# Kernel optimization log

Measured on AMD Instinct MI355X. Metric: run time of the kernel, lower is better.

Reference implementation:

```python
import jax, jax.numpy as jnp
import numpy as np

N = 50000   # nodes
E = 150000  # edges
G = 256     # graphs in batch
H0, H1, H2, H3 = 8, 128, 256, 512


def _lin(key, fi, fo):
    return jax.random.normal(key, (fi, fo), dtype=jnp.float32) * (1.0 / np.sqrt(fi))


def setup_inputs() -> dict:
    key = jax.random.key(0)
    ks = jax.random.split(key, 12)
    x = jax.random.normal(ks[0], (N, H0), dtype=jnp.float32)
    edge_index = jax.random.randint(ks[1], (2, E), 0, N)
    edge_weight = jax.random.uniform(ks[2], (E,), dtype=jnp.float32)
    batch = jnp.sort(jax.random.randint(ks[3], (N,), 0, G))
    return {
        'x': x, 'edge_index': edge_index, 'edge_weight': edge_weight, 'batch': batch,
        'W1': _lin(ks[4], H0, H1), 'b1': jnp.zeros((H1,), jnp.float32),
        'W2': _lin(ks[5], H1, H2), 'b2': jnp.zeros((H2,), jnp.float32),
        'W3': _lin(ks[6], H2, H3), 'b3': jnp.zeros((H3,), jnp.float32),
        'Wfc': _lin(ks[7], H3, 1), 'bfc': jnp.zeros((1,), jnp.float32),
    }


def _gcn_conv(h, W, b, src, dst, ew, n):
    # h: [N, Fin] -> [N, Fout]; symmetric GCN normalization (self-loops already in src/dst/ew)
    h = h @ W                                             # [N, Fout]
    deg = jax.ops.segment_sum(ew, dst, num_segments=n)    # [N]
    dinv = jnp.where(deg > 0, jax.lax.rsqrt(deg), 0.0)
    norm = dinv[src] * ew * dinv[dst]                     # [E+N]
    msgs = h[src] * norm[:, None]                         # gather + scale
    out = jax.ops.segment_sum(msgs, dst, num_segments=n)  # scatter-add
    return out + b


def reference(x, edge_index, edge_weight, batch, W1, b1, W2, b2, W3, b3, Wfc, bfc):
    n = x.shape[0]
    loop = jnp.arange(n)
    src = jnp.concatenate([edge_index[0], loop])
    dst = jnp.concatenate([edge_index[1], loop])
    ew = jnp.concatenate([edge_weight, jnp.ones((n,), edge_weight.dtype)])

    h1 = jax.nn.relu(_gcn_conv(x, W1, b1, src, dst, ew, n))
    h2 = jax.nn.relu(_gcn_conv(h1, W2, b2, src, dst, ew, n))
    h3 = jax.nn.relu(_gcn_conv(h2, W3, b3, src, dst, ew, n))

    # global mean pool over graphs
    sums = jax.ops.segment_sum(h3, batch, num_segments=G)              # [G, H3]
    cnt = jax.ops.segment_sum(jnp.ones((n,), h3.dtype), batch, num_segments=G)
    pooled = sums / jnp.maximum(cnt, 1.0)[:, None]

    return jax.nn.sigmoid(pooled @ Wfc + bfc)              # [G, 1]
```

## Files before the change

### kernel.cpp

```cpp
#include <hip/hip_runtime.h>
#include <math.h>

typedef __attribute__((ext_vector_type(8))) short short8;
typedef __attribute__((ext_vector_type(4))) float floatx4;


__device__ __forceinline__ unsigned short f2bf(float f) {
    unsigned int u = __float_as_uint(f);
    unsigned int r = (u + 0x7fffu + ((u >> 16) & 1u)) >> 16;
    return (unsigned short)r;
}
__device__ __forceinline__ float bfu_lo(unsigned int u) {
    return __uint_as_float(u << 16);
}
__device__ __forceinline__ float bfu_hi(unsigned int u) {
    return __uint_as_float(u & 0xffff0000u);
}


__global__ void k_init_wt(float* __restrict__ deg, int* __restrict__ cnt,
                          int* __restrict__ cursor, int N,
                          const float* __restrict__ W2, unsigned short* __restrict__ WT2,
                          int K2, int F2,
                          const float* __restrict__ W3, unsigned short* __restrict__ WT3,
                          int K3, int F3) {
    int i = blockIdx.x * blockDim.x + threadIdx.x;
    if (i < N) { deg[i] = 1.0f; cnt[i] = 0; cursor[i] = 0; }
    int n2 = K2 * F2;
    if (i < n2) {
        int k = i / F2, n = i % F2;
        WT2[(size_t)n * K2 + k] = f2bf(W2[i]);
    } else {
        int j = i - n2;
        if (j < K3 * F3) {
            int k = j / F3, n = j % F3;
            WT3[(size_t)n * K3 + k] = f2bf(W3[j]);
        }
    }
}

__global__ void k_hist_deg(const int* __restrict__ dst, const float* __restrict__ ew,
                           float* __restrict__ deg, int* __restrict__ cnt, int E) {
    int e = blockIdx.x * blockDim.x + threadIdx.x;
    if (e < E) {
        int d = dst[e];
        atomicAdd(&deg[d], ew[e]);
        atomicAdd(&cnt[d], 1);
    }
}

__global__ __launch_bounds__(256) void k_dinv_scana(float* __restrict__ deg,
                                                    const int* __restrict__ cnt,
                                                    int* __restrict__ bsum, int N) {
    int b = blockIdx.x, t = threadIdx.x;
    int base = b * 1024 + t * 4;
    int s = 0;
#pragma unroll
    for (int j = 0; j < 4; ++j) {
        int i = base + j;
        if (i < N) { deg[i] = rsqrtf(deg[i]); s += cnt[i]; }
    }
    __shared__ int sh[256];
    sh[t] = s; __syncthreads();
    for (int st = 128; st > 0; st >>= 1) { if (t < st) sh[t] += sh[t + st]; __syncthreads(); }
    if (t == 0) bsum[b] = sh[0];
}

__global__ __launch_bounds__(256) void k_scan_c(const int* __restrict__ cnt,
                                                const int* __restrict__ bsum,
                                                int* __restrict__ row_start, int N, int nb) {
    int b = blockIdx.x, t = threadIdx.x;
    __shared__ int sh[256];
    __shared__ int boffs;

    if (t < 64) {
        int s = 0;
        for (int i = t; i < b; i += 64) s += bsum[i];
#pragma unroll
        for (int off = 32; off > 0; off >>= 1) s += __shfl_down(s, off);
        if (t == 0) boffs = s;
    }
    __syncthreads();

    int base = b * 1024 + t * 4;
    int v[4]; int s = 0;
#pragma unroll
    for (int j = 0; j < 4; ++j) { int i = base + j; v[j] = (i < N) ? cnt[i] : 0; s += v[j]; }
    sh[t] = s; __syncthreads();
    for (int off = 1; off < 256; off <<= 1) {
        int x = (t >= off) ? sh[t - off] : 0;
        __syncthreads();
        sh[t] += x;
        __syncthreads();
    }
    int excl = sh[t] - s + boffs;
#pragma unroll
    for (int j = 0; j < 4; ++j) {
        int i = base + j;
        if (i < N) row_start[i] = excl;
        excl += v[j];
        if (i == N - 1) row_start[N] = excl;
    }
}

__global__ void k_scatter_norm(const int* __restrict__ src, const int* __restrict__ dst,
                               const float* __restrict__ ew, const float* __restrict__ dinv,
                               const int* __restrict__ row_start, int* __restrict__ cursor,
                               int* __restrict__ esrc, float* __restrict__ enorm, int E) {
    int e = blockIdx.x * blockDim.x + threadIdx.x;
    if (e >= E) return;
    int d = dst[e], s = src[e];
    int pos = row_start[d] + atomicAdd(&cursor[d], 1);
    esrc[pos] = s;
    enorm[pos] = dinv[s] * ew[e] * dinv[d];
}


__global__ __launch_bounds__(256) void k_l1_gemm(
    const float* __restrict__ x, const float* __restrict__ dinv,
    const int* __restrict__ esrc, const float* __restrict__ enorm,
    const int* __restrict__ row_start, const float* __restrict__ W1,
    const float* __restrict__ b1, unsigned short* __restrict__ h1, int N) {
    __shared__ float As[8][132];
    __shared__ float Bs[8][128];

    int tid = threadIdx.x;
    int bm = blockIdx.x * 128;

#pragma unroll
    for (int i = tid; i < 1024; i += 256) Bs[i >> 7][i & 127] = W1[i];

    if (tid < 128) {
        int n = bm + tid;
        float a[8] = {0, 0, 0, 0, 0, 0, 0, 0};
        if (n < N) {
            float dv = dinv[n];
            float dv2 = dv * dv;
            float4 v0 = *(const float4*)&x[(size_t)n * 8];
            float4 v1 = *(const float4*)&x[(size_t)n * 8 + 4];
            a[0] = v0.x * dv2; a[1] = v0.y * dv2; a[2] = v0.z * dv2; a[3] = v0.w * dv2;
            a[4] = v1.x * dv2; a[5] = v1.y * dv2; a[6] = v1.z * dv2; a[7] = v1.w * dv2;
            int j1 = row_start[n + 1];
            for (int j = row_start[n]; j < j1; ++j) {
                int s = esrc[j];
                float w = enorm[j];
                float4 u0 = *(const float4*)&x[(size_t)s * 8];
                float4 u1 = *(const float4*)&x[(size_t)s * 8 + 4];
                a[0] += w * u0.x; a[1] += w * u0.y; a[2] += w * u0.z; a[3] += w * u0.w;
                a[4] += w * u1.x; a[5] += w * u1.y; a[6] += w * u1.z; a[7] += w * u1.w;
            }
        }
#pragma unroll
        for (int k = 0; k < 8; ++k) As[k][tid] = a[k];
    }
    __syncthreads();

    int tx = tid & 15;
    int ty = tid >> 4;
    float acc[8][8];
#pragma unroll
    for (int i = 0; i < 8; ++i)
#pragma unroll
        for (int j = 0; j < 8; ++j) acc[i][j] = 0.f;

#pragma unroll
    for (int k = 0; k < 8; ++k) {
        float a[8], b[8];
        float4 a0 = *(const float4*)&As[k][ty * 4];
        float4 a1 = *(const float4*)&As[k][ty * 4 + 64];
        float4 b0 = *(const float4*)&Bs[k][tx * 4];
        float4 b1 = *(const float4*)&Bs[k][tx * 4 + 64];
        a[0] = a0.x; a[1] = a0.y; a[2] = a0.z; a[3] = a0.w;
        a[4] = a1.x; a[5] = a1.y; a[6] = a1.z; a[7] = a1.w;
        b[0] = b0.x; b[1] = b0.y; b[2] = b0.z; b[3] = b0.w;
        b[4] = b1.x; b[5] = b1.y; b[6] = b1.z; b[7] = b1.w;
#pragma unroll
        for (int i = 0; i < 8; ++i)
#pragma unroll
            for (int j = 0; j < 8; ++j) acc[i][j] += a[i] * b[j];
    }

    float4 bi0 = *(const float4*)&b1[tx * 4];
    float4 bi1 = *(const float4*)&b1[tx * 4 + 64];
    float bb[8] = {bi0.x, bi0.y, bi0.z, bi0.w, bi1.x, bi1.y, bi1.z, bi1.w};
#pragma unroll
    for (int i = 0; i < 8; ++i) {
        int gm = bm + ((i < 4) ? (ty * 4 + i) : (64 + ty * 4 + i - 4));
        if (gm >= N) continue;
        ushort4 v0, v1;
        v0.x = f2bf(fmaxf(acc[i][0] + bb[0], 0.f));
        v0.y = f2bf(fmaxf(acc[i][1] + bb[1], 0.f));
        v0.z = f2bf(fmaxf(acc[i][2] + bb[2], 0.f));
        v0.w = f2bf(fmaxf(acc[i][3] + bb[3], 0.f));
        v1.x = f2bf(fmaxf(acc[i][4] + bb[4], 0.f));
        v1.y = f2bf(fmaxf(acc[i][5] + bb[5], 0.f));
        v1.z = f2bf(fmaxf(acc[i][6] + bb[6], 0.f));
        v1.w = f2bf(fmaxf(acc[i][7] + bb[7], 0.f));
        *(ushort4*)&h1[(size_t)gm * 128 + tx * 4] = v0;
        *(ushort4*)&h1[(size_t)gm * 128 + tx * 4 + 64] = v1;
    }
}


__global__ void k_agg_bf(const unsigned short* __restrict__ h, const float* __restrict__ dinv,
                         const int* __restrict__ esrc, const float* __restrict__ enorm,
                         const int* __restrict__ row_start,
                         unsigned short* __restrict__ A,
                         int N, int Mpad, int F, int osh) {
    int p = blockIdx.x * blockDim.x + threadIdx.x;
    int oct = F >> 3;
    if (p >= Mpad * oct) return;
    int n = p >> osh;
    int fo = (p & (oct - 1)) << 3;
    size_t oidx = (size_t)n * F + fo;
    if (n >= N) {
        *(uint4*)&A[oidx] = make_uint4(0, 0, 0, 0);
        return;
    }
    float dv = dinv[n];
    float dv2 = dv * dv;
    uint4 hv = *(const uint4*)&h[oidx];
    float s0 = bfu_lo(hv.x) * dv2, s1 = bfu_hi(hv.x) * dv2;
    float s2 = bfu_lo(hv.y) * dv2, s3 = bfu_hi(hv.y) * dv2;
    float s4 = bfu_lo(hv.z) * dv2, s5 = bfu_hi(hv.z) * dv2;
    float s6 = bfu_lo(hv.w) * dv2, s7 = bfu_hi(hv.w) * dv2;
    int j1 = row_start[n + 1];
    for (int j = row_start[n]; j < j1; ++j) {
        int s = esrc[j];
        float w = enorm[j];
        uint4 nv = *(const uint4*)&h[(size_t)s * F + fo];
        s0 += w * bfu_lo(nv.x); s1 += w * bfu_hi(nv.x);
        s2 += w * bfu_lo(nv.y); s3 += w * bfu_hi(nv.y);
        s4 += w * bfu_lo(nv.z); s5 += w * bfu_hi(nv.z);
        s6 += w * bfu_lo(nv.w); s7 += w * bfu_hi(nv.w);
    }
    uint4 o;
    o.x = (unsigned int)f2bf(s0) | ((unsigned int)f2bf(s1) << 16);
    o.y = (unsigned int)f2bf(s2) | ((unsigned int)f2bf(s3) << 16);
    o.z = (unsigned int)f2bf(s4) | ((unsigned int)f2bf(s5) << 16);
    o.w = (unsigned int)f2bf(s6) | ((unsigned int)f2bf(s7) << 16);
    *(uint4*)&A[oidx] = o;
}


template <int EPI>
__global__ __launch_bounds__(256, 4) void k_gemm_async(
    const unsigned short* __restrict__ A, const unsigned short* __restrict__ B,
    const float* __restrict__ bias, unsigned short* __restrict__ C,
    const float* __restrict__ Wfc, float* __restrict__ part,
    int M, int Mpad, int K, int Fout, int nbsh) {
    __shared__ __align__(16) unsigned short smem[8192];

    int tid = threadIdx.x, wave = tid >> 6, lane = tid & 63;
    int quad = lane >> 4, r = lane & 15;

    int P = blockIdx.x;
    int r8 = P & 7;
    int q = P >> 3;
    int bnIdx = q & ((1 << nbsh) - 1);
    int g = ((q >> nbsh) << 3) + r8;
    int bm = g * 128, bn = bnIdx * 128;
    int wm = (wave & 1) * 64, wn = (wave >> 1) * 64;

    const unsigned short* gsrc[2] = {A, B};
    const int rb[2] = {bm, bn};

    floatx4 acc[4][4] = {};

    for (int k0 = 0; k0 < K; k0 += 32) {
#pragma unroll
        for (int t = 0; t < 2; ++t) {
#pragma unroll
            for (int i = 0; i < 2; ++i) {
                int qc = wave * 2 + i;
                int idx = qc * 64 + lane;
                int row = idx >> 2, kofs = (idx & 3) << 3;
                const unsigned short* gptr = gsrc[t] + ((size_t)(rb[t] + row) * K + k0 + kofs);
                unsigned short* l = &smem[t * 4096 + qc * 512];
                __builtin_amdgcn_global_load_lds(
                    (const __attribute__((address_space(1))) void*)gptr,
                    (__attribute__((address_space(3))) void*)l, 16, 0, 0);
            }
        }
        __syncthreads();

        short8 ah[4];
#pragma unroll
        for (int mt = 0; mt < 4; ++mt) {
            int m = wm + mt * 16 + r;
            ah[mt] = *(const short8*)&smem[m * 32 + quad * 8];
        }
#pragma unroll
        for (int nt = 0; nt < 4; ++nt) {
            int n = wn + nt * 16 + r;
            short8 bh = *(const short8*)&smem[4096 + n * 32 + quad * 8];
#pragma unroll
            for (int mt = 0; mt < 4; ++mt)
                acc[mt][nt] = __builtin_amdgcn_mfma_f32_16x16x32_bf16(ah[mt], bh, acc[mt][nt], 0, 0, 0);
        }
        __syncthreads();
    }

    float bv[4];
#pragma unroll
    for (int nt = 0; nt < 4; ++nt) bv[nt] = bias[bn + wn + nt * 16 + r];

    if (EPI == 0) {
        float* eps = (float*)&smem[0] + wave * 1024;
#pragma unroll
        for (int mt = 0; mt < 4; ++mt) {
#pragma unroll
            for (int nt = 0; nt < 4; ++nt)
#pragma unroll
                for (int reg = 0; reg < 4; ++reg)
                    eps[(quad * 4 + reg) * 64 + nt * 16 + r] =
                        fmaxf(acc[mt][nt][reg] + bv[nt], 0.f);
#pragma unroll
            for (int i = 0; i < 4; ++i) {
                int fl = i * 64 + lane;
                int ri = fl >> 4, c4 = fl & 15;
                float4 v = *(const float4*)&eps[ri * 64 + c4 * 4];
                int gm = bm + wm + mt * 16 + ri;
                if (gm < M)
                    *(ushort4*)&C[(size_t)gm * Fout + bn + wn + c4 * 4] =
                        make_ushort4(f2bf(v.x), f2bf(v.y), f2bf(v.z), f2bf(v.w));
            }
        }
    } else {
        float* rowsum = (float*)&smem[0];
        if (tid < 128) rowsum[tid] = 0.f;
        __syncthreads();
        float wf[4];
#pragma unroll
        for (int nt = 0; nt < 4; ++nt) wf[nt] = Wfc[bn + wn + nt * 16 + r];
#pragma unroll
        for (int mt = 0; mt < 4; ++mt)
#pragma unroll
            for (int reg = 0; reg < 4; ++reg) {
                float v = 0.f;
#pragma unroll
                for (int nt = 0; nt < 4; ++nt)
                    v += fmaxf(acc[mt][nt][reg] + bv[nt], 0.f) * wf[nt];
                v += __shfl_xor(v, 1);
                v += __shfl_xor(v, 2);
                v += __shfl_xor(v, 4);
                v += __shfl_xor(v, 8);
                if (r == 0) atomicAdd(&rowsum[wm + mt * 16 + quad * 4 + reg], v);
            }
        __syncthreads();
        if (tid < 128) part[(size_t)bnIdx * Mpad + bm + tid] = rowsum[tid];
    }
}


__global__ __launch_bounds__(256) void k_pool2(const float* __restrict__ part,
                                               const int* __restrict__ batch,
                                               const float* __restrict__ bfc,
                                               float* __restrict__ out,
                                               int N, int Mpad, int nchunks, int G) {
    int g = (int)((blockIdx.x * blockDim.x + threadIdx.x) >> 6);
    int lane = threadIdx.x & 63;
    if (g >= G) return;
    int lo = 0, hi = N;
    while (lo < hi) { int m = (lo + hi) >> 1; if (batch[m] < g) lo = m + 1; else hi = m; }
    int start = lo;
    hi = N;
    while (lo < hi) { int m = (lo + hi) >> 1; if (batch[m] < g + 1) lo = m + 1; else hi = m; }
    int end = lo;
    float s = 0.f;
    for (int i = start + lane; i < end; i += 64) {
        float t = 0.f;
        for (int c = 0; c < nchunks; ++c) t += part[(size_t)c * Mpad + i];
        s += t;
    }
#pragma unroll
    for (int off = 32; off > 0; off >>= 1) s += __shfl_down(s, off);
    if (lane == 0) {
        float c = (float)(end - start);
        if (c < 1.f) c = 1.f;
        float z = s / c + bfc[0];
        out[g] = 1.f / (1.f + expf(-z));
    }
}


static inline int cdiv(int a, int b) { return (a + b - 1) / b; }

extern "C" void kernel_launch(void* const* d_in, const int* in_sizes, int n_in,
                              void* d_out, int out_size, void* d_ws, size_t ws_size,
                              hipStream_t stream) {
    const float* x   = (const float*)d_in[0];
    const int*   ei  = (const int*)d_in[1];
    const float* ew  = (const float*)d_in[2];
    const int*   bat = (const int*)d_in[3];
    const float* W1  = (const float*)d_in[4];
    const float* b1  = (const float*)d_in[5];
    const float* W2  = (const float*)d_in[6];
    const float* b2  = (const float*)d_in[7];
    const float* W3  = (const float*)d_in[8];
    const float* b3  = (const float*)d_in[9];
    const float* Wfc = (const float*)d_in[10];
    const float* bfc = (const float*)d_in[11];
    float* out = (float*)d_out;

    const int N  = in_sizes[3];
    const int E  = in_sizes[2];
    const int H1 = in_sizes[5];
    const int H2 = in_sizes[7];
    const int H3 = in_sizes[9];
    const int G  = out_size;
    const int Mpad = cdiv(N, 1024) * 1024;
    const int Npad4 = (N + 4) & ~3;

    const int* srcv = ei;
    const int* dstv = ei + E;

    char* p = (char*)d_ws;
    float* dinv      = (float*)p; p += (size_t)N * 4;
    int*   cnt       = (int*)p;   p += (size_t)N * 4;
    int*   cursor    = (int*)p;   p += (size_t)N * 4;
    int*   bsum      = (int*)p;   p += 256 * 4;
    int*   row_start = (int*)p;   p += (size_t)Npad4 * 4;
    int*   esrc      = (int*)p;   p += (size_t)E * 4;
    float* enorm     = (float*)p; p += (size_t)E * 4;
    float* part      = (float*)p; p += (size_t)(H3 / 128) * Mpad * 4;
    unsigned short* WT2 = (unsigned short*)p; p += (size_t)H1 * H2 * 2;
    unsigned short* WT3 = (unsigned short*)p; p += (size_t)H2 * H3 * 2;
    unsigned short* Abf = (unsigned short*)p; p += (size_t)Mpad * H2 * 2;
    unsigned short* h1  = (unsigned short*)p; p += (size_t)Mpad * H1 * 2;
    unsigned short* h2  = (unsigned short*)p; p += (size_t)Mpad * H2 * 2;

    int initTot = H1 * H2 + H2 * H3;
    if (initTot < N) initTot = N;
    k_init_wt<<<cdiv(initTot, 256), 256, 0, stream>>>(dinv, cnt, cursor, N,
                                                      W2, WT2, H1, H2, W3, WT3, H2, H3);
    k_hist_deg<<<cdiv(E, 256), 256, 0, stream>>>(dstv, ew, dinv, cnt, E);
    int nb = cdiv(N, 1024);
    k_dinv_scana<<<nb, 256, 0, stream>>>(dinv, cnt, bsum, N);
    k_scan_c<<<nb, 256, 0, stream>>>(cnt, bsum, row_start, N, nb);
    k_scatter_norm<<<cdiv(E, 256), 256, 0, stream>>>(srcv, dstv, ew, dinv, row_start,
                                                     cursor, esrc, enorm, E);

    k_l1_gemm<<<cdiv(N, 128), 256, 0, stream>>>(x, dinv, esrc, enorm, row_start, W1, b1, h1, N);

    k_agg_bf<<<cdiv(Mpad * (H1 / 8), 256), 256, 0, stream>>>(
        h1, dinv, esrc, enorm, row_start, Abf, N, Mpad, H1, __builtin_ctz(H1) - 3);
    k_gemm_async<0><<<(Mpad / 128) * (H2 / 128), 256, 0, stream>>>(
        Abf, WT2, b2, h2, nullptr, nullptr, N, Mpad, H1, H2, __builtin_ctz(H2 / 128));

    k_agg_bf<<<cdiv(Mpad * (H2 / 8), 256), 256, 0, stream>>>(
        h2, dinv, esrc, enorm, row_start, Abf, N, Mpad, H2, __builtin_ctz(H2) - 3);
    k_gemm_async<1><<<(Mpad / 128) * (H3 / 128), 256, 0, stream>>>(
        Abf, WT3, b3, nullptr, Wfc, part, N, Mpad, H2, H3, __builtin_ctz(H3 / 128));

    k_pool2<<<cdiv(G * 64, 256), 256, 0, stream>>>(part, bat, bfc, out, N, Mpad, H3 / 128, G);
}
```

Before: 225.0 us.

## Fuse mean-pool into final GEMM epilogue and unroll edge gathers by four

```diff
diff --git a/kernel.cpp b/kernel.cpp
--- a/kernel.cpp
+++ b/kernel.cpp
@@ -23,9 +23,12 @@
                           const float* __restrict__ W2, unsigned short* __restrict__ WT2,
                           int K2, int F2,
                           const float* __restrict__ W3, unsigned short* __restrict__ WT3,
-                          int K3, int F3) {
+                          int K3, int F3,
+                          float* __restrict__ gsum, int* __restrict__ done, int G) {
     int i = blockIdx.x * blockDim.x + threadIdx.x;
     if (i < N) { deg[i] = 1.0f; cnt[i] = 0; cursor[i] = 0; }
+    if (i < G) gsum[i] = 0.f;
+    if (i == 0) *done = 0;
     int n2 = K2 * F2;
     if (i < n2) {
         int k = i / F2, n = i % F2;
@@ -140,14 +143,32 @@
             float4 v1 = *(const float4*)&x[(size_t)n * 8 + 4];
             a[0] = v0.x * dv2; a[1] = v0.y * dv2; a[2] = v0.z * dv2; a[3] = v0.w * dv2;
             a[4] = v1.x * dv2; a[5] = v1.y * dv2; a[6] = v1.z * dv2; a[7] = v1.w * dv2;
-            int j1 = row_start[n + 1];
-            for (int j = row_start[n]; j < j1; ++j) {
-                int s = esrc[j];
-                float w = enorm[j];
-                float4 u0 = *(const float4*)&x[(size_t)s * 8];
-                float4 u1 = *(const float4*)&x[(size_t)s * 8 + 4];
-                a[0] += w * u0.x; a[1] += w * u0.y; a[2] += w * u0.z; a[3] += w * u0.w;
-                a[4] += w * u1.x; a[5] += w * u1.y; a[6] += w * u1.z; a[7] += w * u1.w;
+            int j0 = row_start[n], j1 = row_start[n + 1];
+            for (int b = j0; b < j1; b += 4) {
+                int i1 = (b + 1 < j1) ? b + 1 : b;
+                int i2 = (b + 2 < j1) ? b + 2 : b;
+                int i3 = (b + 3 < j1) ? b + 3 : b;
+                float w0 = enorm[b];
+                float w1 = (b + 1 < j1) ? enorm[i1] : 0.f;
+                float w2 = (b + 2 < j1) ? enorm[i2] : 0.f;
+                float w3 = (b + 3 < j1) ? enorm[i3] : 0.f;
+                int s0 = esrc[b], s1 = esrc[i1], s2 = esrc[i2], s3 = esrc[i3];
+                float4 p0 = *(const float4*)&x[(size_t)s0 * 8];
+                float4 q0 = *(const float4*)&x[(size_t)s0 * 8 + 4];
+                float4 p1 = *(const float4*)&x[(size_t)s1 * 8];
+                float4 q1 = *(const float4*)&x[(size_t)s1 * 8 + 4];
+                float4 p2 = *(const float4*)&x[(size_t)s2 * 8];
+                float4 q2 = *(const float4*)&x[(size_t)s2 * 8 + 4];
+                float4 p3 = *(const float4*)&x[(size_t)s3 * 8];
+                float4 q3 = *(const float4*)&x[(size_t)s3 * 8 + 4];
+                a[0] += w0 * p0.x + w1 * p1.x + w2 * p2.x + w3 * p3.x;
+                a[1] += w0 * p0.y + w1 * p1.y + w2 * p2.y + w3 * p3.y;
+                a[2] += w0 * p0.z + w1 * p1.z + w2 * p2.z + w3 * p3.z;
+                a[3] += w0 * p0.w + w1 * p1.w + w2 * p2.w + w3 * p3.w;
+                a[4] += w0 * q0.x + w1 * q1.x + w2 * q2.x + w3 * q3.x;
+                a[5] += w0 * q0.y + w1 * q1.y + w2 * q2.y + w3 * q3.y;
+                a[6] += w0 * q0.z + w1 * q1.z + w2 * q2.z + w3 * q3.z;
+                a[7] += w0 * q0.w + w1 * q1.w + w2 * q2.w + w3 * q3.w;
             }
         }
 #pragma unroll
@@ -224,15 +245,28 @@
     float s2 = bfu_lo(hv.y) * dv2, s3 = bfu_hi(hv.y) * dv2;
     float s4 = bfu_lo(hv.z) * dv2, s5 = bfu_hi(hv.z) * dv2;
     float s6 = bfu_lo(hv.w) * dv2, s7 = bfu_hi(hv.w) * dv2;
-    int j1 = row_start[n + 1];
-    for (int j = row_start[n]; j < j1; ++j) {
-        int s = esrc[j];
-        float w = enorm[j];
-        uint4 nv = *(const uint4*)&h[(size_t)s * F + fo];
-        s0 += w * bfu_lo(nv.x); s1 += w * bfu_hi(nv.x);
-        s2 += w * bfu_lo(nv.y); s3 += w * bfu_hi(nv.y);
-        s4 += w * bfu_lo(nv.z); s5 += w * bfu_hi(nv.z);
-        s6 += w * bfu_lo(nv.w); s7 += w * bfu_hi(nv.w);
+    int j0 = row_start[n], j1 = row_start[n + 1];
+    for (int b = j0; b < j1; b += 4) {
+        int i1 = (b + 1 < j1) ? b + 1 : b;
+        int i2 = (b + 2 < j1) ? b + 2 : b;
+        int i3 = (b + 3 < j1) ? b + 3 : b;
+        float w0 = enorm[b];
+        float w1 = (b + 1 < j1) ? enorm[i1] : 0.f;
+        float w2 = (b + 2 < j1) ? enorm[i2] : 0.f;
+        float w3 = (b + 3 < j1) ? enorm[i3] : 0.f;
+        int e0 = esrc[b], e1 = esrc[i1], e2 = esrc[i2], e3 = esrc[i3];
+        uint4 r0 = *(const uint4*)&h[(size_t)e0 * F + fo];
+        uint4 r1 = *(const uint4*)&h[(size_t)e1 * F + fo];
+        uint4 r2 = *(const uint4*)&h[(size_t)e2 * F + fo];
+        uint4 r3 = *(const uint4*)&h[(size_t)e3 * F + fo];
+        s0 += w0 * bfu_lo(r0.x) + w1 * bfu_lo(r1.x) + w2 * bfu_lo(r2.x) + w3 * bfu_lo(r3.x);
+        s1 += w0 * bfu_hi(r0.x) + w1 * bfu_hi(r1.x) + w2 * bfu_hi(r2.x) + w3 * bfu_hi(r3.x);
+        s2 += w0 * bfu_lo(r0.y) + w1 * bfu_lo(r1.y) + w2 * bfu_lo(r2.y) + w3 * bfu_lo(r3.y);
+        s3 += w0 * bfu_hi(r0.y) + w1 * bfu_hi(r1.y) + w2 * bfu_hi(r2.y) + w3 * bfu_hi(r3.y);
+        s4 += w0 * bfu_lo(r0.z) + w1 * bfu_lo(r1.z) + w2 * bfu_lo(r2.z) + w3 * bfu_lo(r3.z);
+        s5 += w0 * bfu_hi(r0.z) + w1 * bfu_hi(r1.z) + w2 * bfu_hi(r2.z) + w3 * bfu_hi(r3.z);
+        s6 += w0 * bfu_lo(r0.w) + w1 * bfu_lo(r1.w) + w2 * bfu_lo(r2.w) + w3 * bfu_lo(r3.w);
+        s7 += w0 * bfu_hi(r0.w) + w1 * bfu_hi(r1.w) + w2 * bfu_hi(r2.w) + w3 * bfu_hi(r3.w);
     }
     uint4 o;
     o.x = (unsigned int)f2bf(s0) | ((unsigned int)f2bf(s1) << 16);
@@ -247,9 +281,12 @@
 __global__ __launch_bounds__(256, 4) void k_gemm_async(
     const unsigned short* __restrict__ A, const unsigned short* __restrict__ B,
     const float* __restrict__ bias, unsigned short* __restrict__ C,
-    const float* __restrict__ Wfc, float* __restrict__ part,
-    int M, int Mpad, int K, int Fout, int nbsh) {
+    const float* __restrict__ Wfc, const int* __restrict__ batch,
+    float* __restrict__ gsum, int* __restrict__ done,
+    const float* __restrict__ bfc, float* __restrict__ outp,
+    int M, int Mpad, int K, int Fout, int nbsh, int G, int nblocks) {
     __shared__ __align__(16) unsigned short smem[8192];
+    __shared__ int lastFlag;
 
     int tid = threadIdx.x, wave = tid >> 6, lane = tid & 63;
     int quad = lane >> 4, r = lane & 15;
@@ -328,6 +365,7 @@
         }
     } else {
         float* rowsum = (float*)&smem[0];
+        int* gsh = (int*)&smem[0] + 128;
         if (tid < 128) rowsum[tid] = 0.f;
         __syncthreads();
         float wf[4];
@@ -347,39 +385,38 @@
                 v += __shfl_xor(v, 8);
                 if (r == 0) atomicAdd(&rowsum[wm + mt * 16 + quad * 4 + reg], v);
             }
-        __syncthreads();
-        if (tid < 128) part[(size_t)bnIdx * Mpad + bm + tid] = rowsum[tid];
-    }
-}
-
-
-__global__ __launch_bounds__(256) void k_pool2(const float* __restrict__ part,
-                                               const int* __restrict__ batch,
-                                               const float* __restrict__ bfc,
-                                               float* __restrict__ out,
-                                               int N, int Mpad, int nchunks, int G) {
-    int g = (int)((blockIdx.x * blockDim.x + threadIdx.x) >> 6);
-    int lane = threadIdx.x & 63;
-    if (g >= G) return;
-    int lo = 0, hi = N;
-    while (lo < hi) { int m = (lo + hi) >> 1; if (batch[m] < g) lo = m + 1; else hi = m; }
-    int start = lo;
-    hi = N;
-    while (lo < hi) { int m = (lo + hi) >> 1; if (batch[m] < g + 1) lo = m + 1; else hi = m; }
-    int end = lo;
-    float s = 0.f;
-    for (int i = start + lane; i < end; i += 64) {
-        float t = 0.f;
-        for (int c = 0; c < nchunks; ++c) t += part[(size_t)c * Mpad + i];
-        s += t;
-    }
-#pragma unroll
-    for (int off = 32; off > 0; off >>= 1) s += __shfl_down(s, off);
-    if (lane == 0) {
-        float c = (float)(end - start);
-        if (c < 1.f) c = 1.f;
-        float z = s / c + bfc[0];
-        out[g] = 1.f / (1.f + expf(-z));
+        if (tid < 128) {
+            int gm = bm + tid;
+            gsh[tid] = (gm < M) ? batch[gm] : -1;
+        }
+        __syncthreads();
+        if (tid < 128) {
+            int gg = gsh[tid];
+            if (gg >= 0 && (tid == 0 || gsh[tid - 1] != gg)) {
+                float s = 0.f;
+                int t2 = tid;
+                while (t2 < 128 && gsh[t2] == gg) { s += rowsum[t2]; ++t2; }
+                atomicAdd(&gsum[gg], s);
+            }
+        }
+        __threadfence();
+        __syncthreads();
+        if (tid == 0) lastFlag = (atomicAdd(done, 1) == nblocks - 1) ? 1 : 0;
+        __syncthreads();
+        if (lastFlag) {
+            for (int gi = tid; gi < G; gi += 256) {
+                int lo = 0, hi = M;
+                while (lo < hi) { int m = (lo + hi) >> 1; if (batch[m] < gi) lo = m + 1; else hi = m; }
+                int start = lo;
+                hi = M;
+                while (lo < hi) { int m = (lo + hi) >> 1; if (batch[m] < gi + 1) lo = m + 1; else hi = m; }
+                float c = (float)(lo - start);
+                if (c < 1.f) c = 1.f;
+                float s = atomicAdd(&gsum[gi], 0.f);
+                float z = s / c + bfc[0];
+                outp[gi] = 1.f / (1.f + expf(-z));
+            }
+        }
     }
 }
 
@@ -423,7 +460,8 @@
     int*   row_start = (int*)p;   p += (size_t)Npad4 * 4;
     int*   esrc      = (int*)p;   p += (size_t)E * 4;
     float* enorm     = (float*)p; p += (size_t)E * 4;
-    float* part      = (float*)p; p += (size_t)(H3 / 128) * Mpad * 4;
+    float* gsum      = (float*)p; p += (size_t)G * 4;
+    int*   done      = (int*)p;   p += 16;
     unsigned short* WT2 = (unsigned short*)p; p += (size_t)H1 * H2 * 2;
     unsigned short* WT3 = (unsigned short*)p; p += (size_t)H2 * H3 * 2;
     unsigned short* Abf = (unsigned short*)p; p += (size_t)Mpad * H2 * 2;
@@ -433,7 +471,8 @@
     int initTot = H1 * H2 + H2 * H3;
     if (initTot < N) initTot = N;
     k_init_wt<<<cdiv(initTot, 256), 256, 0, stream>>>(dinv, cnt, cursor, N,
-                                                      W2, WT2, H1, H2, W3, WT3, H2, H3);
+                                                      W2, WT2, H1, H2, W3, WT3, H2, H3,
+                                                      gsum, done, G);
     k_hist_deg<<<cdiv(E, 256), 256, 0, stream>>>(dstv, ew, dinv, cnt, E);
     int nb = cdiv(N, 1024);
     k_dinv_scana<<<nb, 256, 0, stream>>>(dinv, cnt, bsum, N);
@@ -446,12 +485,13 @@
     k_agg_bf<<<cdiv(Mpad * (H1 / 8), 256), 256, 0, stream>>>(
         h1, dinv, esrc, enorm, row_start, Abf, N, Mpad, H1, __builtin_ctz(H1) - 3);
     k_gemm_async<0><<<(Mpad / 128) * (H2 / 128), 256, 0, stream>>>(
-        Abf, WT2, b2, h2, nullptr, nullptr, N, Mpad, H1, H2, __builtin_ctz(H2 / 128));
+        Abf, WT2, b2, h2, nullptr, nullptr, nullptr, nullptr, nullptr, nullptr,
+        N, Mpad, H1, H2, __builtin_ctz(H2 / 128), G, 0);
 
     k_agg_bf<<<cdiv(Mpad * (H2 / 8), 256), 256, 0, stream>>>(
         h2, dinv, esrc, enorm, row_start, Abf, N, Mpad, H2, __builtin_ctz(H2) - 3);
-    k_gemm_async<1><<<(Mpad / 128) * (H3 / 128), 256, 0, stream>>>(
-        Abf, WT3, b3, nullptr, Wfc, part, N, Mpad, H2, H3, __builtin_ctz(H3 / 128));
-
-    k_pool2<<<cdiv(G * 64, 256), 256, 0, stream>>>(part, bat, bfc, out, N, Mpad, H3 / 128, G);
-}
+    int nblocks3 = (Mpad / 128) * (H3 / 128);
+    k_gemm_async<1><<<nblocks3, 256, 0, stream>>>(
+        Abf, WT3, b3, nullptr, Wfc, bat, gsum, done, bfc, out,
+        N, Mpad, H2, H3, __builtin_ctz(H3 / 128), G, nblocks3);
+}
```

After: 301.9 us. +34.2%, slower.
